# Performance work log

Hardware: AMD Instinct MI355X
Metric: run time of the kernel (lower is better)

The kernel has to match this reference:

```python
import jax, jax.numpy as jnp
import numpy as np

B, T1, H, P, V = 4096, 65, 64, 50, 32
D = H + P  # input_size = 114


def setup_inputs() -> dict:
    key = jax.random.key(0)
    ks = jax.random.split(key, 20)
    s = 1.0 / np.sqrt(D)
    sh = 1.0 / np.sqrt(H)
    inp = {
        "phonetic_input": jax.random.normal(ks[0], (B, P), dtype=jnp.float32),
        "char_seq": jax.random.randint(ks[1], (B, T1), 0, V, dtype=jnp.int64),
        "emb": jax.random.normal(ks[2], (V, H), dtype=jnp.float32).at[0].set(0.0),  # padding_idx=0
        "W_rx": jax.random.uniform(ks[3], (D, H), jnp.float32, -s, s),
        "b_rx": jax.random.uniform(ks[4], (H,), jnp.float32, -s, s),
        "W_rh": jax.random.uniform(ks[5], (H, H), jnp.float32, -sh, sh),
        "b_rh": jax.random.uniform(ks[6], (H,), jnp.float32, -sh, sh),
        "W_zx": jax.random.uniform(ks[7], (D, H), jnp.float32, -s, s),
        "b_zx": jax.random.uniform(ks[8], (H,), jnp.float32, -s, s),
        "W_zh": jax.random.uniform(ks[9], (H, H), jnp.float32, -sh, sh),
        "b_zh": jax.random.uniform(ks[10], (H,), jnp.float32, -sh, sh),
        "W_hx": jax.random.uniform(ks[11], (D, H), jnp.float32, -s, s),
        "b_hx": jax.random.uniform(ks[12], (H,), jnp.float32, -s, s),
        "W_hh": jax.random.uniform(ks[13], (H, H), jnp.float32, -sh, sh),
        "b_hh": jax.random.uniform(ks[14], (H,), jnp.float32, -sh, sh),
        "W_proj": jax.random.uniform(ks[15], (H, V), jnp.float32, -sh, sh),
        "b_proj": jax.random.uniform(ks[16], (V,), jnp.float32, -sh, sh),
    }
    return inp


def reference(phonetic_input, char_seq, emb, W_rx, b_rx, W_rh, b_rh, W_zx, b_zx,
              W_zh, b_zh, W_hx, b_hx, W_hh, b_hh, W_proj, b_proj):
    input_seq = char_seq[:, :-1]          # [B, T]
    target_seq = char_seq[:, 1:]          # [B, T]
    Bsz, T = input_seq.shape

    char_emb = emb[input_seq]                                   # [B, T, H]
    phon = jnp.broadcast_to(phonetic_input[:, None, :], (Bsz, T, P))
    x = jnp.concatenate([char_emb, phon], axis=2)               # [B, T, D]

    # Hoist input-side projections into batched GEMMs, [T, B, H] for scan
    xr = jnp.einsum('btd,dh->tbh', x, W_rx) + b_rx
    xz = jnp.einsum('btd,dh->tbh', x, W_zx) + b_zx
    xh = jnp.einsum('btd,dh->tbh', x, W_hx) + b_hx

    h0 = jnp.zeros((Bsz, H), dtype=x.dtype)

    def step(h, inputs):
        xr_t, xz_t, xh_t = inputs
        r = jax.nn.sigmoid(xr_t + h @ W_rh + b_rh)
        z = jax.nn.sigmoid(xz_t + h @ W_zh + b_zh)
        c = jnp.tanh(xh_t + (r * h) @ W_hh + b_hh)
        h_new = (1.0 - z) * h + z * c
        return h_new, h_new

    _, hs = jax.lax.scan(step, h0, (xr, xz, xh))                # [T, B, H]
    logits = jnp.einsum('tbh,hv->btv', hs, W_proj) + b_proj     # [B, T, V]

    # cross_entropy with ignore_index=0 (mean over non-ignored)
    targets = target_seq.reshape(-1)
    logp = jax.nn.log_softmax(logits.reshape(-1, V), axis=-1)
    nll = -jnp.take_along_axis(logp, targets[:, None], axis=-1)[:, 0]
    mask = (targets != 0).astype(logits.dtype)
    loss = jnp.sum(nll * mask) / jnp.maximum(jnp.sum(mask), 1.0)
    return logits, loss
```

## Files before the change

kernel.cpp:

```cpp
#include <hip/hip_runtime.h>
#include <stdint.h>

#define Bsz 4096
#define Tn  64
#define T1n 65
#define Hn  64
#define Pn  50
#define Vn  32
#define RPB 8

typedef __attribute__((ext_vector_type(8))) short short8;
typedef __attribute__((ext_vector_type(4))) float floatx4;

__device__ __forceinline__ float bf2f(unsigned short u) {
  union { unsigned int i; float f; } x; x.i = ((unsigned int)u) << 16; return x.f;
}
__device__ __forceinline__ unsigned short f2bf(float f) {
  union { float f; unsigned int i; } x; x.f = f;
  return (unsigned short)((x.i + 0x7FFFu + ((x.i >> 16) & 1u)) >> 16);
}
__device__ __forceinline__ float fast_sigmoid(float x) {
  return __builtin_amdgcn_rcpf(1.f + __expf(-x));
}
__device__ __forceinline__ float fast_tanh(float x) {
  return 1.f - 2.f * __builtin_amdgcn_rcpf(1.f + __expf(2.f * x));
}

__device__ __forceinline__ short8 load_bfrag(const float* __restrict__ W, int ncols, int col, int kbase) {
  short8 f;
#pragma unroll
  for (int j = 0; j < 8; ++j) f[j] = (short)f2bf(W[(long)(kbase + j) * ncols + col]);
  return f;
}

__launch_bounds__(256)
__global__ void gru_kernel(const float* __restrict__ phon,
                           const int* __restrict__ cs,
                           const float* __restrict__ emb,
                           const float* __restrict__ Wrx, const float* __restrict__ brx,
                           const float* __restrict__ Wrh, const float* __restrict__ brh,
                           const float* __restrict__ Wzx, const float* __restrict__ bzx,
                           const float* __restrict__ Wzh, const float* __restrict__ bzh,
                           const float* __restrict__ Whx, const float* __restrict__ bhx,
                           const float* __restrict__ Whh, const float* __restrict__ bhh,
                           const float* __restrict__ Wpj, const float* __restrict__ bpj_g,
                           float* __restrict__ ws,
                           float* __restrict__ outp) {
  __shared__ unsigned short tbl_s[3 * 32 * 66];
  __shared__ __align__(16) unsigned short hist_s[16 * 1152];
  __shared__ __align__(16) unsigned short rh_s[16 * 72];
  __shared__ unsigned char code_s[16 * 68];
  __shared__ unsigned short emb_s[32 * 64];
  __shared__ unsigned short ph_s[16 * 52];
  __shared__ int det_s[1];
  __shared__ float red_s[8];

  const int tid = threadIdx.x;
  const int b0 = blockIdx.x * RPB;
  const int w = tid >> 6, lane = tid & 63, q = lane >> 4, c16 = lane & 15;
  const int jcol = w * 16 + c16;

  if (tid == 0) det_s[0] = 0;
  __syncthreads();
  if (tid < 128 && cs[2 * tid + 1] != 0) atomicOr(&det_s[0], 1);
  __syncthreads();
  const bool is64 = (det_s[0] == 0);

  for (int i = tid; i < 16 * 72; i += 256) hist_s[15 * 1152 + i] = 0;
  for (int i = tid; i < 32 * 64; i += 256) emb_s[i] = f2bf(emb[i]);
  for (int i = tid; i < 16 * Pn; i += 256) {
    int m = i / Pn, p = i - m * Pn;
    int mc = (m < RPB) ? m : RPB - 1;
    ph_s[m * 52 + p] = f2bf(phon[(long)(b0 + mc) * Pn + p]);
  }
  for (int i = tid; i < 16 * T1n; i += 256) {
    int m = i / T1n, t = i - m * T1n;
    int mc = (m < RPB) ? m : RPB - 1;
    long idx = (long)(b0 + mc) * T1n + t;
    int c = is64 ? cs[2 * idx] : cs[idx];
    code_s[m * 68 + t] = (unsigned char)c;
  }

  short8 Brh0 = load_bfrag(Wrh, Hn, jcol, q * 8);
  short8 Brh1 = load_bfrag(Wrh, Hn, jcol, 32 + q * 8);
  short8 Bzh0 = load_bfrag(Wzh, Hn, jcol, q * 8);
  short8 Bzh1 = load_bfrag(Wzh, Hn, jcol, 32 + q * 8);
  short8 Bhh0 = load_bfrag(Whh, Hn, jcol, q * 8);
  short8 Bhh1 = load_bfrag(Whh, Hn, jcol, 32 + q * 8);
  short8 Bp00 = load_bfrag(Wpj, Vn, c16,      q * 8);
  short8 Bp01 = load_bfrag(Wpj, Vn, c16,      32 + q * 8);
  short8 Bp10 = load_bfrag(Wpj, Vn, 16 + c16, q * 8);
  short8 Bp11 = load_bfrag(Wpj, Vn, 16 + c16, 32 + q * 8);
  const float bpj0 = bpj_g[c16], bpj1 = bpj_g[16 + c16];

  __syncthreads();

  for (int g = 0; g < 3; ++g) {
    const float* W  = (g == 0) ? Wrx : (g == 1) ? Wzx : Whx;
    const float* bx = (g == 0) ? brx : (g == 1) ? bzx : bhx;
    const float* bh = (g == 0) ? brh : (g == 1) ? bzh : bhh;
    float acc[8] = {0.f, 0.f, 0.f, 0.f, 0.f, 0.f, 0.f, 0.f};
    float bias = bx[lane] + bh[lane];
    for (int d = 0; d < Hn; ++d) {
      float wv = W[(long)d * Hn + lane];
#pragma unroll
      for (int k = 0; k < 8; ++k)
        acc[k] += bf2f(emb_s[(w + 4 * k) * Hn + d]) * wv;
    }
#pragma unroll
    for (int k = 0; k < 8; ++k)
      tbl_s[g * 2112 + (w + 4 * k) * 66 + lane] = f2bf(acc[k] + bias);
  }

  float ph_r[4] = {0.f, 0.f, 0.f, 0.f};
  float ph_z[4] = {0.f, 0.f, 0.f, 0.f};
  float ph_h[4] = {0.f, 0.f, 0.f, 0.f};
  for (int p = 0; p < Pn; ++p) {
    float wr = Wrx[(long)(Hn + p) * Hn + jcol];
    float wz = Wzx[(long)(Hn + p) * Hn + jcol];
    float wh = Whx[(long)(Hn + p) * Hn + jcol];
#pragma unroll
    for (int r = 0; r < 4; ++r) {
      float xv = bf2f(ph_s[(q * 4 + r) * 52 + p]);
      ph_r[r] += xv * wr; ph_z[r] += xv * wz; ph_h[r] += xv * wh;
    }
  }

  float h[4] = {0.f, 0.f, 0.f, 0.f};
  float nll_acc = 0.f, cnt_acc = 0.f;

  __syncthreads();

  for (int qi = 0; qi < 4; ++qi) {
    for (int tt = 0; tt < 16; ++tt) {
      const int t = qi * 16 + tt;
      int cr[4];
#pragma unroll
      for (int r = 0; r < 4; ++r) cr[r] = code_s[(q * 4 + r) * 68 + t];

      const unsigned short* hp = &hist_s[((tt + 15) & 15) * 1152];
      short8 a0 = *(const short8*)&hp[c16 * 72 + q * 8];
      short8 a1 = *(const short8*)&hp[c16 * 72 + 32 + q * 8];
      floatx4 accr = {0.f, 0.f, 0.f, 0.f}, accz = {0.f, 0.f, 0.f, 0.f};
      accr = __builtin_amdgcn_mfma_f32_16x16x32_bf16(a0, Brh0, accr, 0, 0, 0);
      accr = __builtin_amdgcn_mfma_f32_16x16x32_bf16(a1, Brh1, accr, 0, 0, 0);
      accz = __builtin_amdgcn_mfma_f32_16x16x32_bf16(a0, Bzh0, accz, 0, 0, 0);
      accz = __builtin_amdgcn_mfma_f32_16x16x32_bf16(a1, Bzh1, accz, 0, 0, 0);
      float z[4];
#pragma unroll
      for (int r = 0; r < 4; ++r) {
        float xr = bf2f(tbl_s[0 * 2112 + cr[r] * 66 + jcol]) + ph_r[r] + accr[r];
        float rr = fast_sigmoid(xr);
        float xz = bf2f(tbl_s[1 * 2112 + cr[r] * 66 + jcol]) + ph_z[r] + accz[r];
        z[r] = fast_sigmoid(xz);
        rh_s[(q * 4 + r) * 72 + jcol] = f2bf(rr * h[r]);
      }
      __syncthreads();

      short8 p0 = *(const short8*)&rh_s[c16 * 72 + q * 8];
      short8 p1 = *(const short8*)&rh_s[c16 * 72 + 32 + q * 8];
      floatx4 accc = {0.f, 0.f, 0.f, 0.f};
      accc = __builtin_amdgcn_mfma_f32_16x16x32_bf16(p0, Bhh0, accc, 0, 0, 0);
      accc = __builtin_amdgcn_mfma_f32_16x16x32_bf16(p1, Bhh1, accc, 0, 0, 0);
      unsigned short* hw = &hist_s[tt * 1152];
#pragma unroll
      for (int r = 0; r < 4; ++r) {
        float xh = bf2f(tbl_s[2 * 2112 + cr[r] * 66 + jcol]) + ph_h[r] + accc[r];
        float c = fast_tanh(xh);
        float hn = (1.f - z[r]) * h[r] + z[r] * c;
        h[r] = hn;
        hw[(q * 4 + r) * 72 + jcol] = f2bf(hn);
      }
      __syncthreads();
    }

    for (int k = 0; k < 4; ++k) {
      const int tt = k * 4 + w;
      const int t = qi * 16 + tt;
      const unsigned short* hp = &hist_s[tt * 1152];
      const short8 ha0 = *(const short8*)&hp[c16 * 72 + q * 8];
      const short8 ha1 = *(const short8*)&hp[c16 * 72 + 32 + q * 8];
      floatx4 l0 = {0.f, 0.f, 0.f, 0.f}, l1 = {0.f, 0.f, 0.f, 0.f};
      l0 = __builtin_amdgcn_mfma_f32_16x16x32_bf16(ha0, Bp00, l0, 0, 0, 0);
      l0 = __builtin_amdgcn_mfma_f32_16x16x32_bf16(ha1, Bp01, l0, 0, 0, 0);
      l1 = __builtin_amdgcn_mfma_f32_16x16x32_bf16(ha0, Bp10, l1, 0, 0, 0);
      l1 = __builtin_amdgcn_mfma_f32_16x16x32_bf16(ha1, Bp11, l1, 0, 0, 0);
#pragma unroll
      for (int r = 0; r < 4; ++r) {
        int m = q * 4 + r;
        float lg0 = l0[r] + bpj0, lg1 = l1[r] + bpj1;
        float mx = fmaxf(lg0, lg1);
#pragma unroll
        for (int off = 8; off >= 1; off >>= 1) mx = fmaxf(mx, __shfl_xor(mx, off));
        float s = __expf(lg0 - mx) + __expf(lg1 - mx);
#pragma unroll
        for (int off = 8; off >= 1; off >>= 1) s += __shfl_xor(s, off);
        if (m < RPB) {
          float lse = mx + __logf(s);
          long base = (((long)(b0 + m)) * Tn + t) * Vn;
          outp[base + c16] = lg0;
          outp[base + 16 + c16] = lg1;
          int targ = code_s[m * 68 + t + 1];
          if (targ != 0 && c16 == (targ & 15)) {
            float lt = (targ >> 4) ? lg1 : lg0;
            nll_acc += lse - lt; cnt_acc += 1.f;
          }
        }
      }
    }
    __syncthreads();
  }

#pragma unroll
  for (int off = 32; off >= 1; off >>= 1) {
    nll_acc += __shfl_xor(nll_acc, off);
    cnt_acc += __shfl_xor(cnt_acc, off);
  }
  if (lane == 0) { red_s[w] = nll_acc; red_s[4 + w] = cnt_acc; }
  __syncthreads();
  if (tid == 0) {
    ws[2 * blockIdx.x]     = red_s[0] + red_s[1] + red_s[2] + red_s[3];
    ws[2 * blockIdx.x + 1] = red_s[4] + red_s[5] + red_s[6] + red_s[7];
  }
}

__global__ void loss_kernel(const float* __restrict__ ws, float* __restrict__ outp) {
  int lane = threadIdx.x;
  float n = 0.f, c = 0.f;
  for (int i = lane; i < Bsz / RPB; i += 64) { n += ws[2 * i]; c += ws[2 * i + 1]; }
#pragma unroll
  for (int off = 32; off >= 1; off >>= 1) {
    n += __shfl_xor(n, off);
    c += __shfl_xor(c, off);
  }
  if (lane == 0) outp[(size_t)Bsz * Tn * Vn] = n / fmaxf(c, 1.f);
}

extern "C" void kernel_launch(void* const* d_in, const int* in_sizes, int n_in,
                              void* d_out, int out_size, void* d_ws, size_t ws_size,
                              hipStream_t stream) {
  const float* phon = (const float*)d_in[0];
  const int*   cs   = (const int*)d_in[1];
  const float* emb  = (const float*)d_in[2];
  const float* Wrx  = (const float*)d_in[3];
  const float* brx  = (const float*)d_in[4];
  const float* Wrh  = (const float*)d_in[5];
  const float* brh  = (const float*)d_in[6];
  const float* Wzx  = (const float*)d_in[7];
  const float* bzx  = (const float*)d_in[8];
  const float* Wzh  = (const float*)d_in[9];
  const float* bzh  = (const float*)d_in[10];
  const float* Whx  = (const float*)d_in[11];
  const float* bhx  = (const float*)d_in[12];
  const float* Whh  = (const float*)d_in[13];
  const float* bhh  = (const float*)d_in[14];
  const float* Wpj  = (const float*)d_in[15];
  const float* bpj  = (const float*)d_in[16];
  float* ws = (float*)d_ws;

  hipLaunchKernelGGL(gru_kernel, dim3(Bsz / RPB), dim3(256), 0, stream,
                     phon, cs, emb, Wrx, brx, Wrh, brh, Wzx, bzx, Wzh, bzh,
                     Whx, bhx, Whh, bhh, Wpj, bpj, ws, (float*)d_out);
  hipLaunchKernelGGL(loss_kernel, dim3(1), dim3(64), 0, stream, ws, (float*)d_out);
}
```

Before: 207.2 us.

## Warp-specialize GRU block: 16 rows, split gates and pipelined projection

Each block now handles 16 batch rows instead of 8, so the 16-row MFMA tiles are fully used rather than half padded. The block grows to 8 waves. Four waves compute the r gate, the candidate and the h update, while the other four compute the z gate and the output projection for the previous step, with z passed through shared memory. Logits are staged in a shared ring buffer, and softmax/NLL runs every 8 steps; the loss no longer subtracts the max before exponentiating. This is meant to remove redundant MFMA work and move the z gate and projection off the recurrent critical path. In exchange there is one large block per CU, and the log-sum-exp is less numerically safe.

After: 175.1 us. 1.18x faster.

```diff
diff --git a/kernel.cpp b/kernel.cpp
--- a/kernel.cpp
+++ b/kernel.cpp
@@ -7,7 +7,6 @@
 #define Hn  64
 #define Pn  50
 #define Vn  32
-#define RPB 8
 
 typedef __attribute__((ext_vector_type(8))) short short8;
 typedef __attribute__((ext_vector_type(4))) float floatx4;
@@ -33,7 +32,7 @@
   return f;
 }
 
-__launch_bounds__(256)
+__launch_bounds__(512)
 __global__ void gru_kernel(const float* __restrict__ phon,
                            const int* __restrict__ cs,
                            const float* __restrict__ emb,
@@ -47,18 +46,21 @@
                            float* __restrict__ ws,
                            float* __restrict__ outp) {
   __shared__ unsigned short tbl_s[3 * 32 * 66];
-  __shared__ __align__(16) unsigned short hist_s[16 * 1152];
-  __shared__ __align__(16) unsigned short rh_s[16 * 72];
-  __shared__ unsigned char code_s[16 * 68];
-  __shared__ unsigned short emb_s[32 * 64];
-  __shared__ unsigned short ph_s[16 * 52];
+  __shared__ __align__(16) unsigned short hist_s[8 * 1152];
+  __shared__ __align__(16) unsigned short rh_s[1152];
+  __shared__ float z_s[16 * 68];
+  __shared__ float logit_s[8 * 16 * 33];
+  __shared__ unsigned int code4_s[(T1n + 1) * 4];
   __shared__ int det_s[1];
-  __shared__ float red_s[8];
+  __shared__ float red_s[16];
 
   const int tid = threadIdx.x;
-  const int b0 = blockIdx.x * RPB;
-  const int w = tid >> 6, lane = tid & 63, q = lane >> 4, c16 = lane & 15;
+  const int b0 = blockIdx.x * 16;
+  const int W8 = tid >> 6, lane = tid & 63, q = lane >> 4, c16 = lane & 15;
+  const bool isScan = (W8 < 4);
+  const int w = isScan ? W8 : (W8 - 4);
   const int jcol = w * 16 + c16;
+  const floatx4 zf = {0.f, 0.f, 0.f, 0.f};
 
   if (tid == 0) det_s[0] = 0;
   __syncthreads();
@@ -66,168 +68,207 @@
   __syncthreads();
   const bool is64 = (det_s[0] == 0);
 
-  for (int i = tid; i < 16 * 72; i += 256) hist_s[15 * 1152 + i] = 0;
-  for (int i = tid; i < 32 * 64; i += 256) emb_s[i] = f2bf(emb[i]);
-  for (int i = tid; i < 16 * Pn; i += 256) {
-    int m = i / Pn, p = i - m * Pn;
-    int mc = (m < RPB) ? m : RPB - 1;
-    ph_s[m * 52 + p] = f2bf(phon[(long)(b0 + mc) * Pn + p]);
-  }
-  for (int i = tid; i < 16 * T1n; i += 256) {
-    int m = i / T1n, t = i - m * T1n;
-    int mc = (m < RPB) ? m : RPB - 1;
-    long idx = (long)(b0 + mc) * T1n + t;
-    int c = is64 ? cs[2 * idx] : cs[idx];
-    code_s[m * 68 + t] = (unsigned char)c;
-  }
-
-  short8 Brh0 = load_bfrag(Wrh, Hn, jcol, q * 8);
-  short8 Brh1 = load_bfrag(Wrh, Hn, jcol, 32 + q * 8);
-  short8 Bzh0 = load_bfrag(Wzh, Hn, jcol, q * 8);
-  short8 Bzh1 = load_bfrag(Wzh, Hn, jcol, 32 + q * 8);
-  short8 Bhh0 = load_bfrag(Whh, Hn, jcol, q * 8);
-  short8 Bhh1 = load_bfrag(Whh, Hn, jcol, 32 + q * 8);
-  short8 Bp00 = load_bfrag(Wpj, Vn, c16,      q * 8);
-  short8 Bp01 = load_bfrag(Wpj, Vn, c16,      32 + q * 8);
-  short8 Bp10 = load_bfrag(Wpj, Vn, 16 + c16, q * 8);
-  short8 Bp11 = load_bfrag(Wpj, Vn, 16 + c16, 32 + q * 8);
-  const float bpj0 = bpj_g[c16], bpj1 = bpj_g[16 + c16];
-
-  __syncthreads();
+  for (int i = tid; i < 1152; i += 512) hist_s[7 * 1152 + i] = 0;
+  for (int i = tid; i < T1n * 4; i += 512) {
+    int t = i >> 2, qq = i & 3;
+    unsigned int pk = 0;
+#pragma unroll
+    for (int r = 0; r < 4; ++r) {
+      long idx = (long)(b0 + qq * 4 + r) * T1n + t;
+      int c = is64 ? cs[2 * idx] : cs[idx];
+      pk |= ((unsigned int)(c & 255)) << (8 * r);
+    }
+    code4_s[i] = pk;
+  }
 
   for (int g = 0; g < 3; ++g) {
-    const float* W  = (g == 0) ? Wrx : (g == 1) ? Wzx : Whx;
+    const float* Wg = (g == 0) ? Wrx : (g == 1) ? Wzx : Whx;
     const float* bx = (g == 0) ? brx : (g == 1) ? bzx : bhx;
     const float* bh = (g == 0) ? brh : (g == 1) ? bzh : bhh;
-    float acc[8] = {0.f, 0.f, 0.f, 0.f, 0.f, 0.f, 0.f, 0.f};
+    float acc[4] = {0.f, 0.f, 0.f, 0.f};
     float bias = bx[lane] + bh[lane];
     for (int d = 0; d < Hn; ++d) {
-      float wv = W[(long)d * Hn + lane];
-#pragma unroll
-      for (int k = 0; k < 8; ++k)
-        acc[k] += bf2f(emb_s[(w + 4 * k) * Hn + d]) * wv;
-    }
-#pragma unroll
-    for (int k = 0; k < 8; ++k)
-      tbl_s[g * 2112 + (w + 4 * k) * 66 + lane] = f2bf(acc[k] + bias);
-  }
-
-  float ph_r[4] = {0.f, 0.f, 0.f, 0.f};
-  float ph_z[4] = {0.f, 0.f, 0.f, 0.f};
+      float wv = Wg[(long)d * Hn + lane];
+#pragma unroll
+      for (int k = 0; k < 4; ++k)
+        acc[k] += emb[(long)(W8 + 8 * k) * Hn + d] * wv;
+    }
+#pragma unroll
+    for (int k = 0; k < 4; ++k)
+      tbl_s[g * 2112 + (W8 + 8 * k) * 66 + lane] = f2bf(acc[k] + bias);
+  }
+
+  float ph_a[4] = {0.f, 0.f, 0.f, 0.f};
   float ph_h[4] = {0.f, 0.f, 0.f, 0.f};
-  for (int p = 0; p < Pn; ++p) {
-    float wr = Wrx[(long)(Hn + p) * Hn + jcol];
-    float wz = Wzx[(long)(Hn + p) * Hn + jcol];
-    float wh = Whx[(long)(Hn + p) * Hn + jcol];
-#pragma unroll
-    for (int r = 0; r < 4; ++r) {
-      float xv = bf2f(ph_s[(q * 4 + r) * 52 + p]);
-      ph_r[r] += xv * wr; ph_z[r] += xv * wz; ph_h[r] += xv * wh;
+  {
+    const float* Wa = isScan ? Wrx : Wzx;
+    for (int p = 0; p < Pn; ++p) {
+      float wa = Wa[(long)(Hn + p) * Hn + jcol];
+      float wh = isScan ? Whx[(long)(Hn + p) * Hn + jcol] : 0.f;
+#pragma unroll
+      for (int r = 0; r < 4; ++r) {
+        float xv = phon[(long)(b0 + q * 4 + r) * Pn + p];
+        ph_a[r] += xv * wa;
+        ph_h[r] += xv * wh;
+      }
+    }
+  }
+
+  short8 Ba0, Ba1;
+  short8 Bh0, Bh1;
+  short8 Bp0, Bp1;
+  float bpj = 0.f;
+  {
+    const float* Wa = isScan ? Wrh : Wzh;
+    Ba0 = load_bfrag(Wa, Hn, jcol, q * 8);
+    Ba1 = load_bfrag(Wa, Hn, jcol, 32 + q * 8);
+    Bh0 = Ba0; Bh1 = Ba1; Bp0 = Ba0; Bp1 = Ba1;
+    if (isScan) {
+      Bh0 = load_bfrag(Whh, Hn, jcol, q * 8);
+      Bh1 = load_bfrag(Whh, Hn, jcol, 32 + q * 8);
+    } else if (W8 < 6) {
+      int vt = W8 - 4;
+      Bp0 = load_bfrag(Wpj, Vn, vt * 16 + c16, q * 8);
+      Bp1 = load_bfrag(Wpj, Vn, vt * 16 + c16, 32 + q * 8);
+      bpj = bpj_g[vt * 16 + c16];
     }
   }
 
   float h[4] = {0.f, 0.f, 0.f, 0.f};
-  float nll_acc = 0.f, cnt_acc = 0.f;
-
-  __syncthreads();
-
-  for (int qi = 0; qi < 4; ++qi) {
-    for (int tt = 0; tt < 16; ++tt) {
-      const int t = qi * 16 + tt;
-      int cr[4];
-#pragma unroll
-      for (int r = 0; r < 4; ++r) cr[r] = code_s[(q * 4 + r) * 68 + t];
-
-      const unsigned short* hp = &hist_s[((tt + 15) & 15) * 1152];
+  float nll = 0.f, cnt = 0.f;
+
+  __syncthreads();
+
+  for (int t = 0; t < Tn; ++t) {
+    const unsigned int pk = code4_s[t * 4 + q];
+    {
+      const unsigned short* hp = &hist_s[((t + 7) & 7) * 1152];
       short8 a0 = *(const short8*)&hp[c16 * 72 + q * 8];
       short8 a1 = *(const short8*)&hp[c16 * 72 + 32 + q * 8];
-      floatx4 accr = {0.f, 0.f, 0.f, 0.f}, accz = {0.f, 0.f, 0.f, 0.f};
-      accr = __builtin_amdgcn_mfma_f32_16x16x32_bf16(a0, Brh0, accr, 0, 0, 0);
-      accr = __builtin_amdgcn_mfma_f32_16x16x32_bf16(a1, Brh1, accr, 0, 0, 0);
-      accz = __builtin_amdgcn_mfma_f32_16x16x32_bf16(a0, Bzh0, accz, 0, 0, 0);
-      accz = __builtin_amdgcn_mfma_f32_16x16x32_bf16(a1, Bzh1, accz, 0, 0, 0);
-      float z[4];
-#pragma unroll
-      for (int r = 0; r < 4; ++r) {
-        float xr = bf2f(tbl_s[0 * 2112 + cr[r] * 66 + jcol]) + ph_r[r] + accr[r];
-        float rr = fast_sigmoid(xr);
-        float xz = bf2f(tbl_s[1 * 2112 + cr[r] * 66 + jcol]) + ph_z[r] + accz[r];
-        z[r] = fast_sigmoid(xz);
-        rh_s[(q * 4 + r) * 72 + jcol] = f2bf(rr * h[r]);
+      floatx4 acc = __builtin_amdgcn_mfma_f32_16x16x32_bf16(a0, Ba0, zf, 0, 0, 0);
+      acc = __builtin_amdgcn_mfma_f32_16x16x32_bf16(a1, Ba1, acc, 0, 0, 0);
+      if (isScan) {
+#pragma unroll
+        for (int r = 0; r < 4; ++r) {
+          int cr = (pk >> (8 * r)) & 255;
+          float xr = bf2f(tbl_s[0 * 2112 + cr * 66 + jcol]) + ph_a[r] + acc[r];
+          rh_s[(q * 4 + r) * 72 + jcol] = f2bf(fast_sigmoid(xr) * h[r]);
+        }
+      } else {
+#pragma unroll
+        for (int r = 0; r < 4; ++r) {
+          int cr = (pk >> (8 * r)) & 255;
+          float xz = bf2f(tbl_s[1 * 2112 + cr * 66 + jcol]) + ph_a[r] + acc[r];
+          z_s[(q * 4 + r) * 68 + jcol] = fast_sigmoid(xz);
+        }
       }
-      __syncthreads();
-
+    }
+    __syncthreads();
+
+    if (isScan) {
       short8 p0 = *(const short8*)&rh_s[c16 * 72 + q * 8];
       short8 p1 = *(const short8*)&rh_s[c16 * 72 + 32 + q * 8];
-      floatx4 accc = {0.f, 0.f, 0.f, 0.f};
-      accc = __builtin_amdgcn_mfma_f32_16x16x32_bf16(p0, Bhh0, accc, 0, 0, 0);
-      accc = __builtin_amdgcn_mfma_f32_16x16x32_bf16(p1, Bhh1, accc, 0, 0, 0);
-      unsigned short* hw = &hist_s[tt * 1152];
+      floatx4 acc = __builtin_amdgcn_mfma_f32_16x16x32_bf16(p0, Bh0, zf, 0, 0, 0);
+      acc = __builtin_amdgcn_mfma_f32_16x16x32_bf16(p1, Bh1, acc, 0, 0, 0);
+      unsigned short* hw = &hist_s[(t & 7) * 1152];
 #pragma unroll
       for (int r = 0; r < 4; ++r) {
-        float xh = bf2f(tbl_s[2 * 2112 + cr[r] * 66 + jcol]) + ph_h[r] + accc[r];
+        int cr = (pk >> (8 * r)) & 255;
+        float xh = bf2f(tbl_s[2 * 2112 + cr * 66 + jcol]) + ph_h[r] + acc[r];
         float c = fast_tanh(xh);
-        float hn = (1.f - z[r]) * h[r] + z[r] * c;
+        float zr = z_s[(q * 4 + r) * 68 + jcol];
+        float hn = (1.f - zr) * h[r] + zr * c;
         h[r] = hn;
         hw[(q * 4 + r) * 72 + jcol] = f2bf(hn);
       }
-      __syncthreads();
-    }
-
-    for (int k = 0; k < 4; ++k) {
-      const int tt = k * 4 + w;
-      const int t = qi * 16 + tt;
-      const unsigned short* hp = &hist_s[tt * 1152];
-      const short8 ha0 = *(const short8*)&hp[c16 * 72 + q * 8];
-      const short8 ha1 = *(const short8*)&hp[c16 * 72 + 32 + q * 8];
-      floatx4 l0 = {0.f, 0.f, 0.f, 0.f}, l1 = {0.f, 0.f, 0.f, 0.f};
-      l0 = __builtin_amdgcn_mfma_f32_16x16x32_bf16(ha0, Bp00, l0, 0, 0, 0);
-      l0 = __builtin_amdgcn_mfma_f32_16x16x32_bf16(ha1, Bp01, l0, 0, 0, 0);
-      l1 = __builtin_amdgcn_mfma_f32_16x16x32_bf16(ha0, Bp10, l1, 0, 0, 0);
-      l1 = __builtin_amdgcn_mfma_f32_16x16x32_bf16(ha1, Bp11, l1, 0, 0, 0);
-#pragma unroll
-      for (int r = 0; r < 4; ++r) {
-        int m = q * 4 + r;
-        float lg0 = l0[r] + bpj0, lg1 = l1[r] + bpj1;
-        float mx = fmaxf(lg0, lg1);
-#pragma unroll
-        for (int off = 8; off >= 1; off >>= 1) mx = fmaxf(mx, __shfl_xor(mx, off));
-        float s = __expf(lg0 - mx) + __expf(lg1 - mx);
-#pragma unroll
-        for (int off = 8; off >= 1; off >>= 1) s += __shfl_xor(s, off);
-        if (m < RPB) {
-          float lse = mx + __logf(s);
-          long base = (((long)(b0 + m)) * Tn + t) * Vn;
-          outp[base + c16] = lg0;
-          outp[base + 16 + c16] = lg1;
-          int targ = code_s[m * 68 + t + 1];
-          if (targ != 0 && c16 == (targ & 15)) {
-            float lt = (targ >> 4) ? lg1 : lg0;
-            nll_acc += lse - lt; cnt_acc += 1.f;
-          }
+    } else if (W8 < 6 && t > 0) {
+      const unsigned short* hp = &hist_s[((t + 7) & 7) * 1152];
+      short8 a0 = *(const short8*)&hp[c16 * 72 + q * 8];
+      short8 a1 = *(const short8*)&hp[c16 * 72 + 32 + q * 8];
+      floatx4 l = __builtin_amdgcn_mfma_f32_16x16x32_bf16(a0, Bp0, zf, 0, 0, 0);
+      l = __builtin_amdgcn_mfma_f32_16x16x32_bf16(a1, Bp1, l, 0, 0, 0);
+      float* pg = &logit_s[((t - 1) & 7) * 528];
+      int vt = W8 - 4;
+#pragma unroll
+      for (int r = 0; r < 4; ++r)
+        pg[(q * 4 + r) * 33 + vt * 16 + c16] = l[r] + bpj;
+    }
+    __syncthreads();
+
+    if ((t & 7) == 7) {
+      int p = t - 8 + W8;
+      if (p >= 0) {
+        const float* pg = &logit_s[(p & 7) * 528];
+        int v = lane & 31, hf = lane >> 5;
+        unsigned int pk1 = 0;
+#pragma unroll
+        for (int i = 0; i < 8; ++i) {
+          int m = i * 2 + hf;
+          float lg = pg[m * 33 + v];
+          float s = __expf(lg);
+#pragma unroll
+          for (int off = 16; off >= 1; off >>= 1) s += __shfl_xor(s, off);
+          float lse = __logf(s);
+          outp[(((long)(b0 + m)) * Tn + p) * Vn + v] = lg;
+          pk1 = code4_s[(p + 1) * 4 + (m >> 2)];
+          int targ = (pk1 >> (8 * (m & 3))) & 255;
+          if (targ != 0 && v == targ) { nll += lse - lg; cnt += 1.f; }
         }
       }
     }
-    __syncthreads();
+  }
+
+  __syncthreads();
+  if (W8 >= 4 && W8 < 6) {
+    const unsigned short* hp = &hist_s[7 * 1152];
+    short8 a0 = *(const short8*)&hp[c16 * 72 + q * 8];
+    short8 a1 = *(const short8*)&hp[c16 * 72 + 32 + q * 8];
+    floatx4 l = __builtin_amdgcn_mfma_f32_16x16x32_bf16(a0, Bp0, zf, 0, 0, 0);
+    l = __builtin_amdgcn_mfma_f32_16x16x32_bf16(a1, Bp1, l, 0, 0, 0);
+    int vt = W8 - 4;
+#pragma unroll
+    for (int r = 0; r < 4; ++r)
+      logit_s[7 * 528 + (q * 4 + r) * 33 + vt * 16 + c16] = l[r] + bpj;
+  }
+  __syncthreads();
+  if (W8 == 0) {
+    const float* pg = &logit_s[7 * 528];
+    int v = lane & 31, hf = lane >> 5;
+#pragma unroll
+    for (int i = 0; i < 8; ++i) {
+      int m = i * 2 + hf;
+      float lg = pg[m * 33 + v];
+      float s = __expf(lg);
+#pragma unroll
+      for (int off = 16; off >= 1; off >>= 1) s += __shfl_xor(s, off);
+      float lse = __logf(s);
+      outp[(((long)(b0 + m)) * Tn + 63) * Vn + v] = lg;
+      unsigned int pk1 = code4_s[64 * 4 + (m >> 2)];
+      int targ = (pk1 >> (8 * (m & 3))) & 255;
+      if (targ != 0 && v == targ) { nll += lse - lg; cnt += 1.f; }
+    }
   }
 
 #pragma unroll
   for (int off = 32; off >= 1; off >>= 1) {
-    nll_acc += __shfl_xor(nll_acc, off);
-    cnt_acc += __shfl_xor(cnt_acc, off);
-  }
-  if (lane == 0) { red_s[w] = nll_acc; red_s[4 + w] = cnt_acc; }
+    nll += __shfl_xor(nll, off);
+    cnt += __shfl_xor(cnt, off);
+  }
+  if (lane == 0) { red_s[W8] = nll; red_s[8 + W8] = cnt; }
   __syncthreads();
   if (tid == 0) {
-    ws[2 * blockIdx.x]     = red_s[0] + red_s[1] + red_s[2] + red_s[3];
-    ws[2 * blockIdx.x + 1] = red_s[4] + red_s[5] + red_s[6] + red_s[7];
+    float n = 0.f, c = 0.f;
+#pragma unroll
+    for (int i = 0; i < 8; ++i) { n += red_s[i]; c += red_s[8 + i]; }
+    ws[2 * blockIdx.x] = n;
+    ws[2 * blockIdx.x + 1] = c;
   }
 }
 
 __global__ void loss_kernel(const float* __restrict__ ws, float* __restrict__ outp) {
   int lane = threadIdx.x;
   float n = 0.f, c = 0.f;
-  for (int i = lane; i < Bsz / RPB; i += 64) { n += ws[2 * i]; c += ws[2 * i + 1]; }
+  for (int i = lane; i < Bsz / 16; i += 64) { n += ws[2 * i]; c += ws[2 * i + 1]; }
 #pragma unroll
   for (int off = 32; off >= 1; off >>= 1) {
     n += __shfl_xor(n, off);
@@ -258,7 +299,7 @@
   const float* bpj  = (const float*)d_in[16];
   float* ws = (float*)d_ws;
 
-  hipLaunchKernelGGL(gru_kernel, dim3(Bsz / RPB), dim3(256), 0, stream,
+  hipLaunchKernelGGL(gru_kernel, dim3(Bsz / 16), dim3(512), 0, stream,
                      phon, cs, emb, Wrx, brx, Wrh, brh, Wzx, bzx, Wzh, bzh,
                      Whx, bhx, Whh, bhh, Wpj, bpj, ws, (float*)d_out);
   hipLaunchKernelGGL(loss_kernel, dim3(1), dim3(64), 0, stream, ws, (float*)d_out);
```
